# Performance work log

Measured on AMD Instinct MI355X. Metric: run time of the kernel, lower is better.

## Reference

```python
import jax, jax.numpy as jnp
import numpy as np

N_NODES = 50000
N_EDGES = 800000
NFEAT, NHID, NOUT = 256, 256, 128


def setup_inputs() -> dict:
    key = jax.random.key(0)
    ks = jax.random.split(key, 5)
    stdv1 = 1.0 / np.sqrt(NHID)
    stdv2 = 1.0 / np.sqrt(NOUT)
    x = jax.random.normal(ks[0], (N_NODES, NFEAT), dtype=jnp.float32)
    w1 = jax.random.uniform(ks[1], (NFEAT, NHID), minval=-stdv1, maxval=stdv1, dtype=jnp.float32)
    w2 = jax.random.uniform(ks[2], (NHID, NOUT), minval=-stdv2, maxval=stdv2, dtype=jnp.float32)
    edge_src = jax.random.randint(ks[3], (N_EDGES,), 0, N_NODES, dtype=jnp.int32)
    edge_dst = jax.random.randint(ks[4], (N_EDGES,), 0, N_NODES, dtype=jnp.int32)
    return {"x": x, "w1": w1, "w2": w2, "edge_src": edge_src, "edge_dst": edge_dst}


def _gcn_layer(h, w, edge_src, edge_dst, n):
    # support = h @ w ; out[i] = sum_{(src,dst=i) in E} support[src]  (SpMM with 0/1 adj)
    support = jnp.dot(h, w)                      # [N, out]
    return jax.ops.segment_sum(support[edge_src], edge_dst, num_segments=n)


def reference(x, w1, w2, edge_src, edge_dst):
    n = x.shape[0]
    h = jax.nn.relu(_gcn_layer(x, w1, edge_src, edge_dst, n))
    # dropout is identity in eval mode (training=False)
    out = _gcn_layer(h, w2, edge_src, edge_dst, n)
    return out
```

## Files before the change

### kernel.cpp

```cpp
#include <hip/hip_runtime.h>
#include <hip/hip_bf16.h>


#define NFEAT 256
#define NOUT  128
#define SLOT_CAP 64

typedef short short8 __attribute__((ext_vector_type(8)));
typedef float floatx4 __attribute__((ext_vector_type(4)));
typedef float floatx2 __attribute__((ext_vector_type(2)));

typedef const __attribute__((address_space(1))) unsigned short GAS_US;
typedef __attribute__((address_space(3))) unsigned short LAS_US;

__device__ __forceinline__ unsigned short f2bf(float f) {
    unsigned u = __builtin_bit_cast(unsigned, f);
    unsigned r = (u + 0x7FFFu + ((u >> 16) & 1u)) >> 16;
    return (unsigned short)r;
}
__device__ __forceinline__ unsigned char f2fp8(float f) {
    int p = __builtin_amdgcn_cvt_pk_fp8_f32(f, f, 0, false);
    return (unsigned char)(p & 0xFF);
}
__device__ __forceinline__ void accf8(float* a, uint2 v) {
    floatx2 f0 = __builtin_amdgcn_cvt_pk_f32_fp8(v.x, false);
    floatx2 f1 = __builtin_amdgcn_cvt_pk_f32_fp8(v.x, true);
    floatx2 f2 = __builtin_amdgcn_cvt_pk_f32_fp8(v.y, false);
    floatx2 f3 = __builtin_amdgcn_cvt_pk_f32_fp8(v.y, true);
    a[0] += f0.x; a[1] += f0.y; a[2] += f1.x; a[3] += f1.y;
    a[4] += f2.x; a[5] += f2.y; a[6] += f3.x; a[7] += f3.y;
}


__global__ __launch_bounds__(256) void k_prep_w(const float* __restrict__ w1,
                                                const float* __restrict__ w2,
                                                unsigned short* __restrict__ w1T,
                                                unsigned short* __restrict__ w2T,
                                                int* __restrict__ cnt, int n) {
    int b = blockIdx.x;
    if (b < 256) {
        int idx = b * 256 + threadIdx.x;
        int nn = idx >> 8, k = idx & 255;
        w1T[idx] = f2bf(w1[k * 256 + nn]);
        return;
    }
    b -= 256;
    if (b < 128) {
        int idx = b * 256 + threadIdx.x;
        int nn = idx >> 8, k = idx & 255;
        w2T[idx] = f2bf(w2[k * 128 + nn]);
        return;
    }
    b -= 128;
    {
        int i = (b * 256 + threadIdx.x) * 4;
        if (i < n) {
            if (i + 4 <= n) *(int4*)&cnt[i] = make_int4(0, 0, 0, 0);
            else for (int t = i; t < n; ++t) cnt[t] = 0;
        }
    }
}


#define GBM 128
#define GBN 128
#define GBK 64

__global__ __launch_bounds__(256) void k_build_gemm1(
        const float* __restrict__ x,
        const unsigned short* __restrict__ BT,
        unsigned char* __restrict__ C,
        const int* __restrict__ esrc, const int* __restrict__ edst,
        int* __restrict__ cnt, unsigned short* __restrict__ slots,
        int M, int E, int nBuild, int rangeSize) {
    __shared__ unsigned short As[GBM * GBK];
    __shared__ unsigned short Bs[GBN * GBK];

    int b = blockIdx.x;
    if (b < nBuild) {
        int range = b & 7;
        int chunk = b >> 3;
        int lo = range * rangeSize;
        int hi = lo + rangeSize;
        int base = chunk * 2048 + threadIdx.x * 8;
        if (base + 8 <= E) {
            int4 s0 = *(const int4*)&esrc[base];
            int4 s1 = *(const int4*)&esrc[base + 4];
            int4 d0 = *(const int4*)&edst[base];
            int4 d1 = *(const int4*)&edst[base + 4];
            int ss[8] = {s0.x, s0.y, s0.z, s0.w, s1.x, s1.y, s1.z, s1.w};
            int dd[8] = {d0.x, d0.y, d0.z, d0.w, d1.x, d1.y, d1.z, d1.w};
#pragma unroll
            for (int t = 0; t < 8; ++t) {
                int d = dd[t];
                if (d >= lo && d < hi) {
                    int pos = atomicAdd(&cnt[d], 1);
                    if (pos < SLOT_CAP)
                        slots[(size_t)d * SLOT_CAP + pos] = (unsigned short)ss[t];
                }
            }
        } else {
#pragma unroll
            for (int t = 0; t < 8; ++t) {
                int i = base + t;
                if (i < E) {
                    int d = edst[i];
                    if (d >= lo && d < hi) {
                        int pos = atomicAdd(&cnt[d], 1);
                        if (pos < SLOT_CAP)
                            slots[(size_t)d * SLOT_CAP + pos] = (unsigned short)esrc[i];
                    }
                }
            }
        }
        return;
    }

    const int N = 256, K = 256;
    int g = b - nBuild;
    int bx = g >> 1, by = g & 1;
    int tid = threadIdx.x;
    int lane = tid & 63, wave = tid >> 6;
    int wm = (wave >> 1) * 64, wn = (wave & 1) * 64;
    int q = lane >> 4, r = lane & 15;
    int m0 = bx * GBM, n0 = by * GBN;

    int srow = (lane >> 3);
    int scol = (lane & 7) * 8;

    floatx4 acc[4][4];
#pragma unroll
    for (int i = 0; i < 4; ++i)
#pragma unroll
        for (int j = 0; j < 4; ++j) acc[i][j] = (floatx4){0.f, 0.f, 0.f, 0.f};

    for (int k0 = 0; k0 < K; k0 += GBK) {
#pragma unroll
        for (int t = 0; t < 4; ++t) {
            int row = wave * 32 + t * 8 + srow;
            __builtin_amdgcn_global_load_lds(
                (GAS_US*)&BT[(size_t)(n0 + row) * K + k0 + scol],
                (LAS_US*)&Bs[(wave * 32 + t * 8) * GBK], 16, 0, 0);
        }
#pragma unroll
        for (int u = 0; u < 4; ++u) {
            int unit = tid + u * 256;
            int row = unit >> 3, cg = unit & 7;
            int gm = m0 + row; if (gm >= M) gm = M - 1;
            const float* src = &x[(size_t)gm * 256 + k0 + cg * 8];
            float4 f0 = *(const float4*)src;
            float4 f1 = *(const float4*)(src + 4);
            short8 v;
            v[0] = (short)f2bf(f0.x); v[1] = (short)f2bf(f0.y);
            v[2] = (short)f2bf(f0.z); v[3] = (short)f2bf(f0.w);
            v[4] = (short)f2bf(f1.x); v[5] = (short)f2bf(f1.y);
            v[6] = (short)f2bf(f1.z); v[7] = (short)f2bf(f1.w);
            *(short8*)&As[row * GBK + cg * 8] = v;
        }
        __syncthreads();

#pragma unroll
        for (int kk = 0; kk < GBK; kk += 32) {
            short8 af[4], bfr[4];
#pragma unroll
            for (int i = 0; i < 4; ++i)
                af[i] = *(const short8*)&As[(wm + i * 16 + r) * GBK + kk + q * 8];
#pragma unroll
            for (int j = 0; j < 4; ++j)
                bfr[j] = *(const short8*)&Bs[(wn + j * 16 + r) * GBK + kk + q * 8];
#pragma unroll
            for (int i = 0; i < 4; ++i)
#pragma unroll
                for (int j = 0; j < 4; ++j)
                    acc[i][j] = __builtin_amdgcn_mfma_f32_16x16x32_bf16(
                        af[i], bfr[j], acc[i][j], 0, 0, 0);
        }
        __syncthreads();
    }

#pragma unroll
    for (int i = 0; i < 4; ++i) {
#pragma unroll
        for (int rr = 0; rr < 4; ++rr) {
            int grow = m0 + wm + i * 16 + q * 4 + rr;
            if (grow < M) {
                size_t base = (size_t)grow * N + n0 + wn;
#pragma unroll
                for (int j = 0; j < 4; ++j)
                    C[base + j * 16 + r] = f2fp8(acc[i][j][rr]);
            }
        }
    }
}


__global__ __launch_bounds__(256) void k_gemm2(const unsigned short* __restrict__ A,
                                               const unsigned short* __restrict__ BT,
                                               unsigned char* __restrict__ C,
                                               int M, int N, int K) {
    __shared__ unsigned short As[GBM * GBK];
    __shared__ unsigned short Bs[GBN * GBK];
    int tid = threadIdx.x;
    int lane = tid & 63, wave = tid >> 6;
    int wm = (wave >> 1) * 64, wn = (wave & 1) * 64;
    int q = lane >> 4, r = lane & 15;
    int m0 = blockIdx.x * GBM, n0 = blockIdx.y * GBN;

    int srow = (lane >> 3);
    int scol = (lane & 7) * 8;

    floatx4 acc[4][4];
#pragma unroll
    for (int i = 0; i < 4; ++i)
#pragma unroll
        for (int j = 0; j < 4; ++j) acc[i][j] = (floatx4){0.f, 0.f, 0.f, 0.f};

    for (int k0 = 0; k0 < K; k0 += GBK) {
#pragma unroll
        for (int t = 0; t < 4; ++t) {
            int row = wave * 32 + t * 8 + srow;
            int gm = m0 + row; if (gm >= M) gm = M - 1;
            __builtin_amdgcn_global_load_lds(
                (GAS_US*)&A[(size_t)gm * K + k0 + scol],
                (LAS_US*)&As[(wave * 32 + t * 8) * GBK], 16, 0, 0);
            __builtin_amdgcn_global_load_lds(
                (GAS_US*)&BT[(size_t)(n0 + row) * K + k0 + scol],
                (LAS_US*)&Bs[(wave * 32 + t * 8) * GBK], 16, 0, 0);
        }
        __syncthreads();

#pragma unroll
        for (int kk = 0; kk < GBK; kk += 32) {
            short8 af[4], bfr[4];
#pragma unroll
            for (int i = 0; i < 4; ++i)
                af[i] = *(const short8*)&As[(wm + i * 16 + r) * GBK + kk + q * 8];
#pragma unroll
            for (int j = 0; j < 4; ++j)
                bfr[j] = *(const short8*)&Bs[(wn + j * 16 + r) * GBK + kk + q * 8];
#pragma unroll
            for (int i = 0; i < 4; ++i)
#pragma unroll
                for (int j = 0; j < 4; ++j)
                    acc[i][j] = __builtin_amdgcn_mfma_f32_16x16x32_bf16(
                        af[i], bfr[j], acc[i][j], 0, 0, 0);
        }
        __syncthreads();
    }

#pragma unroll
    for (int i = 0; i < 4; ++i) {
#pragma unroll
        for (int rr = 0; rr < 4; ++rr) {
            int grow = m0 + wm + i * 16 + q * 4 + rr;
            if (grow < M) {
                size_t base = (size_t)grow * N + n0 + wn;
#pragma unroll
                for (int j = 0; j < 4; ++j)
                    C[base + j * 16 + r] = f2fp8(acc[i][j][rr]);
            }
        }
    }
}


__global__ __launch_bounds__(256) void k_gather_relu256(const unsigned char* __restrict__ sup,
                                                        const int* __restrict__ cnt,
                                                        const unsigned short* __restrict__ slots,
                                                        unsigned short* __restrict__ h, int n) {
    int lane = threadIdx.x & 63, wave = threadIdx.x >> 6;
    int half = lane >> 5, l32 = lane & 31;
    int node = blockIdx.x * 8 + wave * 2 + half;
    bool valid = node < n;
    int end = valid ? min(cnt[node], SLOT_CAP) : 0;
    const unsigned short* slot = &slots[(size_t)node * SLOT_CAP];
    float a[8] = {};
    int e = 0;
    for (; e + 8 <= end; e += 8) {
        int s[8];
#pragma unroll
        for (int t = 0; t < 8; ++t) s[t] = slot[e + t];
        uint2 v[8];
#pragma unroll
        for (int t = 0; t < 8; ++t)
            v[t] = *(const uint2*)&sup[(size_t)s[t] * 256 + l32 * 8];
#pragma unroll
        for (int t = 0; t < 8; ++t) accf8(a, v[t]);
    }
    for (; e + 4 <= end; e += 4) {
        int s0 = slot[e], s1 = slot[e + 1], s2 = slot[e + 2], s3 = slot[e + 3];
        uint2 v0 = *(const uint2*)&sup[(size_t)s0 * 256 + l32 * 8];
        uint2 v1 = *(const uint2*)&sup[(size_t)s1 * 256 + l32 * 8];
        uint2 v2 = *(const uint2*)&sup[(size_t)s2 * 256 + l32 * 8];
        uint2 v3 = *(const uint2*)&sup[(size_t)s3 * 256 + l32 * 8];
        accf8(a, v0); accf8(a, v1); accf8(a, v2); accf8(a, v3);
    }
    for (; e < end; ++e) {
        uint2 v = *(const uint2*)&sup[(size_t)slot[e] * 256 + l32 * 8];
        accf8(a, v);
    }
    if (valid) {
        uint4 o;
        o.x = (unsigned)f2bf(fmaxf(a[0], 0.f)) | ((unsigned)f2bf(fmaxf(a[1], 0.f)) << 16);
        o.y = (unsigned)f2bf(fmaxf(a[2], 0.f)) | ((unsigned)f2bf(fmaxf(a[3], 0.f)) << 16);
        o.z = (unsigned)f2bf(fmaxf(a[4], 0.f)) | ((unsigned)f2bf(fmaxf(a[5], 0.f)) << 16);
        o.w = (unsigned)f2bf(fmaxf(a[6], 0.f)) | ((unsigned)f2bf(fmaxf(a[7], 0.f)) << 16);
        *(uint4*)&h[(size_t)node * 256 + l32 * 8] = o;
    }
}


__global__ __launch_bounds__(256) void k_gather128(const unsigned char* __restrict__ sup,
                                                   const int* __restrict__ cnt,
                                                   const unsigned short* __restrict__ slots,
                                                   float* __restrict__ outp, int n) {
    int lane = threadIdx.x & 63, wave = threadIdx.x >> 6;
    int quarter = lane >> 4, l16 = lane & 15;
    int node = blockIdx.x * 16 + wave * 4 + quarter;
    bool valid = node < n;
    int end = valid ? min(cnt[node], SLOT_CAP) : 0;
    const unsigned short* slot = &slots[(size_t)node * SLOT_CAP];
    float a[8] = {};
    int e = 0;
    for (; e + 8 <= end; e += 8) {
        int s[8];
#pragma unroll
        for (int t = 0; t < 8; ++t) s[t] = slot[e + t];
        uint2 v[8];
#pragma unroll
        for (int t = 0; t < 8; ++t)
            v[t] = *(const uint2*)&sup[(size_t)s[t] * 128 + l16 * 8];
#pragma unroll
        for (int t = 0; t < 8; ++t) accf8(a, v[t]);
    }
    for (; e + 4 <= end; e += 4) {
        int s0 = slot[e], s1 = slot[e + 1], s2 = slot[e + 2], s3 = slot[e + 3];
        uint2 v0 = *(const uint2*)&sup[(size_t)s0 * 128 + l16 * 8];
        uint2 v1 = *(const uint2*)&sup[(size_t)s1 * 128 + l16 * 8];
        uint2 v2 = *(const uint2*)&sup[(size_t)s2 * 128 + l16 * 8];
        uint2 v3 = *(const uint2*)&sup[(size_t)s3 * 128 + l16 * 8];
        accf8(a, v0); accf8(a, v1); accf8(a, v2); accf8(a, v3);
    }
    for (; e < end; ++e) {
        uint2 v = *(const uint2*)&sup[(size_t)slot[e] * 128 + l16 * 8];
        accf8(a, v);
    }
    if (valid) {
        size_t base = (size_t)node * 128 + l16 * 8;
        *(float4*)&outp[base]     = make_float4(a[0], a[1], a[2], a[3]);
        *(float4*)&outp[base + 4] = make_float4(a[4], a[5], a[6], a[7]);
    }
}


extern "C" void kernel_launch(void* const* d_in, const int* in_sizes, int n_in,
                              void* d_out, int out_size, void* d_ws, size_t ws_size,
                              hipStream_t stream) {
    const float* x    = (const float*)d_in[0];
    const float* w1   = (const float*)d_in[1];
    const float* w2   = (const float*)d_in[2];
    const int*   esrc = (const int*)d_in[3];
    const int*   edst = (const int*)d_in[4];
    float*       out  = (float*)d_out;

    const int N = in_sizes[0] / NFEAT;
    const int E = in_sizes[3];

    char* ws = (char*)d_ws;
    size_t off = 0;
    unsigned short* hb   = (unsigned short*)(ws + off); off += (size_t)N * 256 * 2;
    unsigned char*  sup1 = (unsigned char*)(ws + off);  off += (size_t)N * 256;
    unsigned char*  sup2 = (unsigned char*)(ws + off);  off += (size_t)N * 128;
    unsigned short* w1T  = (unsigned short*)(ws + off); off += (size_t)256 * 256 * 2;
    unsigned short* w2T  = (unsigned short*)(ws + off); off += (size_t)128 * 256 * 2;
    off = (off + 255) & ~(size_t)255;
    int* cnt = (int*)(ws + off); off += (size_t)N * sizeof(int);
    off = (off + 255) & ~(size_t)255;
    unsigned short* slots = (unsigned short*)(ws + off);
    off += (size_t)N * SLOT_CAP * sizeof(unsigned short);
    (void)ws_size; (void)n_in; (void)out_size;

    int bZero = (N + 1023) / 1024;
    k_prep_w<<<256 + 128 + bZero, 256, 0, stream>>>(w1, w2, w1T, w2T, cnt, N);

    {
        int nChunk = (E + 2047) / 2048;
        int nBuild = nChunk * 8;
        int nGemmX = (N + GBM - 1) / GBM;
        int rangeSize = (N + 7) / 8;
        k_build_gemm1<<<nBuild + 2 * nGemmX, 256, 0, stream>>>(
            x, w1T, sup1, esrc, edst, cnt, slots, N, E, nBuild, rangeSize);
    }

    k_gather_relu256<<<(N + 7) / 8, 256, 0, stream>>>(sup1, cnt, slots, hb, N);

    {
        dim3 grid((N + GBM - 1) / GBM, 128 / GBN);
        k_gemm2<<<grid, 256, 0, stream>>>(hb, w2T, sup2, N, 128, 256);
    }
    k_gather128<<<(N + 15) / 16, 256, 0, stream>>>(sup2, cnt, slots, out, N);
}
```

Before: 213.0 us.

## Build exact CSR via two-level binned counting sort instead of fixed-cap slots

Replaces the per-node fixed-capacity slot table, filled by global atomics and with edges beyond 64 dropped, with a counting sort. Edges are first histogrammed per 256-node bin and chunk, the counts are prefix-scanned, and packed (dst,src) pairs are scattered into bins using shared-memory atomics. A per-bin kernel then sorts each bin locally in LDS into a compact CSR with offsets. This removes the global atomic contention and the strided, mostly empty slot reads in the gather kernels, at the cost of three extra kernel launches and an extra pass over the edges. Bins larger than the LDS cap are truncated.

```diff
diff --git a/kernel.cpp b/kernel.cpp
--- a/kernel.cpp
+++ b/kernel.cpp
@@ -4,7 +4,8 @@
 
 #define NFEAT 256
 #define NOUT  128
-#define SLOT_CAP 64
+#define CHUNK 4096
+#define P4CAP 5120
 
 typedef short short8 __attribute__((ext_vector_type(8)));
 typedef float floatx4 __attribute__((ext_vector_type(4)));
@@ -32,33 +33,73 @@
 }
 
 
-__global__ __launch_bounds__(256) void k_prep_w(const float* __restrict__ w1,
-                                                const float* __restrict__ w2,
-                                                unsigned short* __restrict__ w1T,
-                                                unsigned short* __restrict__ w2T,
-                                                int* __restrict__ cnt, int n) {
-    int b = blockIdx.x;
+__global__ __launch_bounds__(256) void k_prep(const float* __restrict__ w1,
+                                              const float* __restrict__ w2,
+                                              unsigned short* __restrict__ w1T,
+                                              unsigned short* __restrict__ w2T,
+                                              const int* __restrict__ edst,
+                                              int* __restrict__ counts_bm,
+                                              int E, int bins, int pblk) {
+    __shared__ int h[256];
+    int b = blockIdx.x, tid = threadIdx.x;
     if (b < 256) {
-        int idx = b * 256 + threadIdx.x;
+        int idx = b * 256 + tid;
         int nn = idx >> 8, k = idx & 255;
         w1T[idx] = f2bf(w1[k * 256 + nn]);
         return;
     }
-    b -= 256;
-    if (b < 128) {
-        int idx = b * 256 + threadIdx.x;
+    if (b < 384) {
+        int idx = (b - 256) * 256 + tid;
         int nn = idx >> 8, k = idx & 255;
         w2T[idx] = f2bf(w2[k * 128 + nn]);
         return;
     }
-    b -= 128;
-    {
-        int i = (b * 256 + threadIdx.x) * 4;
-        if (i < n) {
-            if (i + 4 <= n) *(int4*)&cnt[i] = make_int4(0, 0, 0, 0);
-            else for (int t = i; t < n; ++t) cnt[t] = 0;
-        }
-    }
+    int blk = b - 384;
+    h[tid] = 0;
+    __syncthreads();
+    int base = blk * CHUNK;
+#pragma unroll
+    for (int t = 0; t < CHUNK / 256; ++t) {
+        int i = base + t * 256 + tid;
+        if (i < E) atomicAdd(&h[edst[i] >> 8], 1);
+    }
+    __syncthreads();
+    for (int j = tid; j < bins; j += 256)
+        counts_bm[j * pblk + blk] = h[j];
+}
+
+
+__global__ __launch_bounds__(1024) void k_scan1(const int* __restrict__ deg,
+                                                int* __restrict__ excl,
+                                                int* __restrict__ partials, int n) {
+    __shared__ int s[1024];
+    int gid = blockIdx.x * 1024 + threadIdx.x;
+    int v = (gid < n) ? deg[gid] : 0;
+    s[threadIdx.x] = v;
+    __syncthreads();
+    for (int off = 1; off < 1024; off <<= 1) {
+        int t = (threadIdx.x >= off) ? s[threadIdx.x - off] : 0;
+        __syncthreads();
+        s[threadIdx.x] += t;
+        __syncthreads();
+    }
+    if (gid < n) excl[gid] = s[threadIdx.x] - v;
+    if (threadIdx.x == 1023) partials[blockIdx.x] = s[1023];
+}
+
+__global__ __launch_bounds__(1024) void k_scan3(int* __restrict__ excl,
+                                                const int* __restrict__ partials,
+                                                int n, int total) {
+    __shared__ int pfx;
+    if (threadIdx.x < 64) {
+        int v = ((int)threadIdx.x < (int)blockIdx.x) ? partials[threadIdx.x] : 0;
+        for (int o = 32; o > 0; o >>= 1) v += __shfl_down(v, o, 64);
+        if (threadIdx.x == 0) pfx = v;
+    }
+    __syncthreads();
+    int gid = blockIdx.x * 1024 + threadIdx.x;
+    if (gid < n) excl[gid] += pfx;
+    if (gid == 0) excl[n] = total;
 }
 
 
@@ -66,65 +107,47 @@
 #define GBN 128
 #define GBK 64
 
-__global__ __launch_bounds__(256) void k_build_gemm1(
+__global__ __launch_bounds__(256) void k_gemm1_scatter(
         const float* __restrict__ x,
         const unsigned short* __restrict__ BT,
         unsigned char* __restrict__ C,
         const int* __restrict__ esrc, const int* __restrict__ edst,
-        int* __restrict__ cnt, unsigned short* __restrict__ slots,
-        int M, int E, int nBuild, int rangeSize) {
+        const int* __restrict__ offs_bm,
+        unsigned int* __restrict__ edgePk,
+        int M, int E, int nGemm, int bins, int pblk) {
     __shared__ unsigned short As[GBM * GBK];
     __shared__ unsigned short Bs[GBN * GBK];
-
-    int b = blockIdx.x;
-    if (b < nBuild) {
-        int range = b & 7;
-        int chunk = b >> 3;
-        int lo = range * rangeSize;
-        int hi = lo + rangeSize;
-        int base = chunk * 2048 + threadIdx.x * 8;
-        if (base + 8 <= E) {
-            int4 s0 = *(const int4*)&esrc[base];
-            int4 s1 = *(const int4*)&esrc[base + 4];
-            int4 d0 = *(const int4*)&edst[base];
-            int4 d1 = *(const int4*)&edst[base + 4];
-            int ss[8] = {s0.x, s0.y, s0.z, s0.w, s1.x, s1.y, s1.z, s1.w};
-            int dd[8] = {d0.x, d0.y, d0.z, d0.w, d1.x, d1.y, d1.z, d1.w};
-#pragma unroll
-            for (int t = 0; t < 8; ++t) {
-                int d = dd[t];
-                if (d >= lo && d < hi) {
-                    int pos = atomicAdd(&cnt[d], 1);
-                    if (pos < SLOT_CAP)
-                        slots[(size_t)d * SLOT_CAP + pos] = (unsigned short)ss[t];
-                }
+    int b = blockIdx.x, tid = threadIdx.x;
+
+    if (b >= nGemm) {
+        int blk = b - nGemm;
+        int* baseOff = (int*)As;
+        int* cur     = (int*)Bs;
+        for (int j = tid; j < bins; j += 256) {
+            baseOff[j] = offs_bm[j * pblk + blk];
+            cur[j] = 0;
+        }
+        __syncthreads();
+        int base = blk * CHUNK;
+#pragma unroll
+        for (int t = 0; t < CHUNK / 256; ++t) {
+            int i = base + t * 256 + tid;
+            if (i < E) {
+                int d = edst[i], s = esrc[i];
+                int bin = d >> 8;
+                int pos = atomicAdd(&cur[bin], 1);
+                edgePk[baseOff[bin] + pos] = ((unsigned)d << 16) | (unsigned)s;
             }
-        } else {
-#pragma unroll
-            for (int t = 0; t < 8; ++t) {
-                int i = base + t;
-                if (i < E) {
-                    int d = edst[i];
-                    if (d >= lo && d < hi) {
-                        int pos = atomicAdd(&cnt[d], 1);
-                        if (pos < SLOT_CAP)
-                            slots[(size_t)d * SLOT_CAP + pos] = (unsigned short)esrc[i];
-                    }
-                }
-            }
         }
         return;
     }
 
     const int N = 256, K = 256;
-    int g = b - nBuild;
-    int bx = g >> 1, by = g & 1;
-    int tid = threadIdx.x;
+    int bx = b >> 1, by = b & 1;
     int lane = tid & 63, wave = tid >> 6;
     int wm = (wave >> 1) * 64, wn = (wave & 1) * 64;
     int q = lane >> 4, r = lane & 15;
     int m0 = bx * GBM, n0 = by * GBN;
-
     int srow = (lane >> 3);
     int scol = (lane & 7) * 8;
 
@@ -158,7 +181,6 @@
             *(short8*)&As[row * GBK + cg * 8] = v;
         }
         __syncthreads();
-
 #pragma unroll
         for (int kk = 0; kk < GBK; kk += 32) {
             short8 af[4], bfr[4];
@@ -190,6 +212,51 @@
                     C[base + j * 16 + r] = f2fp8(acc[i][j][rr]);
             }
         }
+    }
+}
+
+
+__global__ __launch_bounds__(256) void k_p4(const unsigned int* __restrict__ edgePk,
+                                            const int* __restrict__ offs_bm,
+                                            unsigned short* __restrict__ csr,
+                                            int* __restrict__ offsets,
+                                            int N, int E, int bins, int pblk) {
+    __shared__ unsigned int buf[P4CAP];
+    __shared__ int h[256], loff[256], cur[256];
+    int b = blockIdx.x, tid = threadIdx.x;
+    int s0 = offs_bm[b * pblk];
+    int s1 = (b + 1 < bins) ? offs_bm[(b + 1) * pblk] : E;
+    int n = s1 - s0; if (n > P4CAP) n = P4CAP;
+    h[tid] = 0;
+    __syncthreads();
+    for (int i = tid; i < n; i += 256) {
+        unsigned int p = edgePk[s0 + i];
+        buf[i] = p;
+        atomicAdd(&h[(p >> 16) & 255], 1);
+    }
+    __syncthreads();
+    int v = h[tid];
+    loff[tid] = v;
+    __syncthreads();
+    for (int off = 1; off < 256; off <<= 1) {
+        int t2 = (tid >= off) ? loff[tid - off] : 0;
+        __syncthreads();
+        loff[tid] += t2;
+        __syncthreads();
+    }
+    int excl = loff[tid] - v;
+    int node = b * 256 + tid;
+    if (node < N) offsets[node] = s0 + excl;
+    if (b == bins - 1 && tid == 0) offsets[N] = E;
+    cur[tid] = 0;
+    __syncthreads();
+    loff[tid] = excl;
+    __syncthreads();
+    for (int i = tid; i < n; i += 256) {
+        unsigned int p = buf[i];
+        int ld = (p >> 16) & 255;
+        int pos = atomicAdd(&cur[ld], 1);
+        csr[s0 + loff[ld] + pos] = (unsigned short)(p & 0xFFFFu);
     }
 }
 
@@ -205,7 +272,6 @@
     int wm = (wave >> 1) * 64, wn = (wave & 1) * 64;
     int q = lane >> 4, r = lane & 15;
     int m0 = blockIdx.x * GBM, n0 = blockIdx.y * GBN;
-
     int srow = (lane >> 3);
     int scol = (lane & 7) * 8;
 
@@ -228,7 +294,6 @@
                 (LAS_US*)&Bs[(wave * 32 + t * 8) * GBK], 16, 0, 0);
         }
         __syncthreads();
-
 #pragma unroll
         for (int kk = 0; kk < GBK; kk += 32) {
             short8 af[4], bfr[4];
@@ -265,18 +330,20 @@
 
 
 __global__ __launch_bounds__(256) void k_gather_relu256(const unsigned char* __restrict__ sup,
-                                                        const int* __restrict__ cnt,
-                                                        const unsigned short* __restrict__ slots,
+                                                        const int* __restrict__ offsets,
+                                                        const unsigned short* __restrict__ csr,
                                                         unsigned short* __restrict__ h, int n) {
     int lane = threadIdx.x & 63, wave = threadIdx.x >> 6;
     int half = lane >> 5, l32 = lane & 31;
     int node = blockIdx.x * 8 + wave * 2 + half;
     bool valid = node < n;
-    int end = valid ? min(cnt[node], SLOT_CAP) : 0;
-    const unsigned short* slot = &slots[(size_t)node * SLOT_CAP];
+    int beg = valid ? offsets[node] : 0;
+    int end = valid ? offsets[node + 1] : 0;
+    int cnt = end - beg;
+    const unsigned short* slot = &csr[beg];
     float a[8] = {};
     int e = 0;
-    for (; e + 8 <= end; e += 8) {
+    for (; e + 8 <= cnt; e += 8) {
         int s[8];
 #pragma unroll
         for (int t = 0; t < 8; ++t) s[t] = slot[e + t];
@@ -287,7 +354,7 @@
 #pragma unroll
         for (int t = 0; t < 8; ++t) accf8(a, v[t]);
     }
-    for (; e + 4 <= end; e += 4) {
+    for (; e + 4 <= cnt; e += 4) {
         int s0 = slot[e], s1 = slot[e + 1], s2 = slot[e + 2], s3 = slot[e + 3];
         uint2 v0 = *(const uint2*)&sup[(size_t)s0 * 256 + l32 * 8];
         uint2 v1 = *(const uint2*)&sup[(size_t)s1 * 256 + l32 * 8];
@@ -295,7 +362,7 @@
         uint2 v3 = *(const uint2*)&sup[(size_t)s3 * 256 + l32 * 8];
         accf8(a, v0); accf8(a, v1); accf8(a, v2); accf8(a, v3);
     }
-    for (; e < end; ++e) {
+    for (; e < cnt; ++e) {
         uint2 v = *(const uint2*)&sup[(size_t)slot[e] * 256 + l32 * 8];
         accf8(a, v);
     }
@@ -311,18 +378,20 @@
 
 
 __global__ __launch_bounds__(256) void k_gather128(const unsigned char* __restrict__ sup,
-                                                   const int* __restrict__ cnt,
-                                                   const unsigned short* __restrict__ slots,
+                                                   const int* __restrict__ offsets,
+                                                   const unsigned short* __restrict__ csr,
                                                    float* __restrict__ outp, int n) {
     int lane = threadIdx.x & 63, wave = threadIdx.x >> 6;
     int quarter = lane >> 4, l16 = lane & 15;
     int node = blockIdx.x * 16 + wave * 4 + quarter;
     bool valid = node < n;
-    int end = valid ? min(cnt[node], SLOT_CAP) : 0;
-    const unsigned short* slot = &slots[(size_t)node * SLOT_CAP];
+    int beg = valid ? offsets[node] : 0;
+    int end = valid ? offsets[node + 1] : 0;
+    int cnt = end - beg;
+    const unsigned short* slot = &csr[beg];
     float a[8] = {};
     int e = 0;
-    for (; e + 8 <= end; e += 8) {
+    for (; e + 8 <= cnt; e += 8) {
         int s[8];
 #pragma unroll
         for (int t = 0; t < 8; ++t) s[t] = slot[e + t];
@@ -333,7 +402,7 @@
 #pragma unroll
         for (int t = 0; t < 8; ++t) accf8(a, v[t]);
     }
-    for (; e + 4 <= end; e += 4) {
+    for (; e + 4 <= cnt; e += 4) {
         int s0 = slot[e], s1 = slot[e + 1], s2 = slot[e + 2], s3 = slot[e + 3];
         uint2 v0 = *(const uint2*)&sup[(size_t)s0 * 128 + l16 * 8];
         uint2 v1 = *(const uint2*)&sup[(size_t)s1 * 128 + l16 * 8];
@@ -341,7 +410,7 @@
         uint2 v3 = *(const uint2*)&sup[(size_t)s3 * 128 + l16 * 8];
         accf8(a, v0); accf8(a, v1); accf8(a, v2); accf8(a, v3);
     }
-    for (; e < end; ++e) {
+    for (; e < cnt; ++e) {
         uint2 v = *(const uint2*)&sup[(size_t)slot[e] * 128 + l16 * 8];
         accf8(a, v);
     }
@@ -366,6 +435,10 @@
     const int N = in_sizes[0] / NFEAT;
     const int E = in_sizes[3];
 
+    const int bins = (N + 255) / 256;
+    const int pblk = (E + CHUNK - 1) / CHUNK;
+    const int nFlat = bins * pblk;
+
     char* ws = (char*)d_ws;
     size_t off = 0;
     unsigned short* hb   = (unsigned short*)(ws + off); off += (size_t)N * 256 * 2;
@@ -374,29 +447,40 @@
     unsigned short* w1T  = (unsigned short*)(ws + off); off += (size_t)256 * 256 * 2;
     unsigned short* w2T  = (unsigned short*)(ws + off); off += (size_t)128 * 256 * 2;
     off = (off + 255) & ~(size_t)255;
-    int* cnt = (int*)(ws + off); off += (size_t)N * sizeof(int);
-    off = (off + 255) & ~(size_t)255;
-    unsigned short* slots = (unsigned short*)(ws + off);
-    off += (size_t)N * SLOT_CAP * sizeof(unsigned short);
+    int* counts_bm = (int*)(ws + off); off += (size_t)nFlat * sizeof(int);
+    off = (off + 255) & ~(size_t)255;
+    int* offs_bm   = (int*)(ws + off); off += ((size_t)nFlat + 1) * sizeof(int);
+    off = (off + 255) & ~(size_t)255;
+    int* partials  = (int*)(ws + off); off += 64 * sizeof(int);
+    off = (off + 255) & ~(size_t)255;
+    unsigned int* edgePk = (unsigned int*)(ws + off); off += (size_t)E * sizeof(unsigned int);
+    off = (off + 255) & ~(size_t)255;
+    unsigned short* csr  = (unsigned short*)(ws + off); off += (size_t)E * sizeof(unsigned short);
+    off = (off + 255) & ~(size_t)255;
+    int* offsets   = (int*)(ws + off); off += ((size_t)N + 1) * sizeof(int);
     (void)ws_size; (void)n_in; (void)out_size;
 
-    int bZero = (N + 1023) / 1024;
-    k_prep_w<<<256 + 128 + bZero, 256, 0, stream>>>(w1, w2, w1T, w2T, cnt, N);
+    k_prep<<<384 + pblk, 256, 0, stream>>>(w1, w2, w1T, w2T, edst, counts_bm,
+                                           E, bins, pblk);
+
+    int nb = (nFlat + 1023) / 1024;
+    k_scan1<<<nb, 1024, 0, stream>>>(counts_bm, offs_bm, partials, nFlat);
+    k_scan3<<<nb, 1024, 0, stream>>>(offs_bm, partials, nFlat, E);
 
     {
-        int nChunk = (E + 2047) / 2048;
-        int nBuild = nChunk * 8;
-        int nGemmX = (N + GBM - 1) / GBM;
-        int rangeSize = (N + 7) / 8;
-        k_build_gemm1<<<nBuild + 2 * nGemmX, 256, 0, stream>>>(
-            x, w1T, sup1, esrc, edst, cnt, slots, N, E, nBuild, rangeSize);
-    }
-
-    k_gather_relu256<<<(N + 7) / 8, 256, 0, stream>>>(sup1, cnt, slots, hb, N);
+        int nGemm = 2 * ((N + GBM - 1) / GBM);
+        k_gemm1_scatter<<<nGemm + pblk, 256, 0, stream>>>(
+            x, w1T, sup1, esrc, edst, offs_bm, edgePk, N, E, nGemm, bins, pblk);
+    }
+
+    k_p4<<<bins, 256, 0, stream>>>(edgePk, offs_bm, csr, offsets, N, E, bins, pblk);
+
+    k_gather_relu256<<<(N + 7) / 8, 256, 0, stream>>>(sup1, offsets, csr, hb, N);
 
     {
         dim3 grid((N + GBM - 1) / GBM, 128 / GBN);
         k_gemm2<<<grid, 256, 0, stream>>>(hb, w2T, sup2, N, 128, 256);
     }
-    k_gather128<<<(N + 15) / 16, 256, 0, stream>>>(sup2, cnt, slots, out, N);
-}
+
+    k_gather128<<<(N + 15) / 16, 256, 0, stream>>>(sup2, offsets, csr, out, N);
+}
```

Measured after the change: 196.5 us. 1.08x faster.
